# Kernel optimization log

Hardware: AMD Instinct MI355X
Metric: run time of the kernel (lower is better)

The kernel has to match this reference:

```python
import jax, jax.numpy as jnp
import numpy as np

B, T, N, D, H, C = 32, 64, 22, 512, 8, 128
DEPTH = D // H


def setup_inputs() -> dict:
    key = jax.random.key(0)
    ks = jax.random.split(key, 10)
    s = 0.02
    return {
        "x": jax.random.normal(ks[0], (B, T, N, D), jnp.float32),
        "context": jax.random.normal(ks[1], (B, C, D), jnp.float32),
        "Wq": jax.random.normal(ks[2], (N, D, D), jnp.float32) * s,  # per-joint Q proj
        "bq": jax.random.normal(ks[3], (N, D), jnp.float32) * s,
        "Wk": jax.random.normal(ks[4], (D, D), jnp.float32) * s,
        "bk": jax.random.normal(ks[5], (D,), jnp.float32) * s,
        "Wv": jax.random.normal(ks[6], (D, D), jnp.float32) * s,
        "bv": jax.random.normal(ks[7], (D,), jnp.float32) * s,
        "Wout": jax.random.normal(ks[8], (D, D), jnp.float32) * s,
        "bout": jax.random.normal(ks[9], (D,), jnp.float32) * s,
    }


def reference(x, context, Wq, bq, Wk, bk, Wv, bv, Wout, bout):
    b, t, n, d = x.shape
    c = context.shape[1]
    h, dh = H, DEPTH
    # Per-joint Q projection fused into one batched GEMM: [B,T,N,D] x [N,D,D] -> [B,T,N,D]
    q = jnp.einsum('btnd,ndf->btnf', x, Wq) + bq  # bq broadcasts over (B,T)
    # Shared K/V computed ONCE (original recomputes per joint; math identical)
    k = context @ Wk + bk  # [B,C,D]
    v = context @ Wv + bv  # [B,C,D]
    # Split heads
    qh = q.reshape(b, t, n, h, dh)
    kh = k.reshape(b, c, h, dh)
    vh = v.reshape(b, c, h, dh)
    scale = 1.0 / float(np.sqrt(dh))
    # Attention logits per joint: [B,N,H,T,C]
    logits = jnp.einsum('btnhd,bchd->bnhtc', qh, kh) * scale
    attn = jax.nn.softmax(logits, axis=-1)
    # Attend shared V, merge heads: [B,T,N,D]
    o = jnp.einsum('bnhtc,bchd->btnhd', attn, vh).reshape(b, t, n, d)
    # Shared output projection
    return o @ Wout + bout
```

## Files before the change

kernel.cpp:

```cpp
#include <hip/hip_runtime.h>
#include <hip/hip_bf16.h>

#define NB 32
#define NT 64
#define NJ 22
#define ND 512
#define NH 8
#define NC 128
#define NDH 64
#define NR 1408

typedef __attribute__((ext_vector_type(8))) short s16x8;
typedef __attribute__((ext_vector_type(4))) float fx4;

static __device__ __forceinline__ unsigned short f2bf(float f) {
    unsigned u = __builtin_bit_cast(unsigned, f);
    u += 0x7fffu + ((u >> 16) & 1u);
    return (unsigned short)(u >> 16);
}

static __device__ __forceinline__ fx4 mfma16(s16x8 a, s16x8 b, fx4 c) {
    return __builtin_amdgcn_mfma_f32_16x16x32_bf16(a, b, c, 0, 0, 0);
}

static __device__ __forceinline__ void gload16(const void* g, void* l) {
    __builtin_amdgcn_global_load_lds(
        (const __attribute__((address_space(1))) void*)g,
        (__attribute__((address_space(3))) void*)l,
        16, 0, 0);
}

template <int DIV>
__global__ __launch_bounds__(256) void convswz_k(const float* __restrict__ src,
                                                 unsigned short* __restrict__ dst)
{
    const long i = ((long)blockIdx.x * 256 + threadIdx.x) * 8;
    const unsigned row = (unsigned)(i >> 9);
    const int  key = (int)((row / (unsigned)DIV) & 7u);
    const int  c   = (int)((i >> 3) & 7);
    const int  cs  = c ^ key;
    const long j   = (i & ~63L) | ((long)cs << 3);
    const float4 a = *reinterpret_cast<const float4*>(src + i);
    const float4 b = *reinterpret_cast<const float4*>(src + i + 4);
    unsigned short t[8];
    t[0]=f2bf(a.x); t[1]=f2bf(a.y); t[2]=f2bf(a.z); t[3]=f2bf(a.w);
    t[4]=f2bf(b.x); t[5]=f2bf(b.y); t[6]=f2bf(b.z); t[7]=f2bf(b.w);
    *reinterpret_cast<s16x8*>(dst + j) = *reinterpret_cast<s16x8*>(t);
}

__global__ __launch_bounds__(256) void twconv_k(const float* __restrict__ W,
                                                unsigned short* __restrict__ Wt,
                                                long zsrc, long zdst)
{
    __shared__ float T[64][65];
    const int tid = threadIdx.x;
    W  += blockIdx.z * zsrc + (long)blockIdx.x * 64 * 512 + blockIdx.y * 64;
    Wt += blockIdx.z * zdst + (long)blockIdx.y * 64 * 512 + blockIdx.x * 64;
    const int r = tid >> 2, c0 = (tid & 3) * 16;
    #pragma unroll
    for (int i = 0; i < 4; ++i) {
        const float4 p = *reinterpret_cast<const float4*>(W + (long)r * 512 + c0 + i*4);
        T[r][c0 + i*4 + 0] = p.x; T[r][c0 + i*4 + 1] = p.y;
        T[r][c0 + i*4 + 2] = p.z; T[r][c0 + i*4 + 3] = p.w;
    }
    __syncthreads();
    unsigned short o[16];
    #pragma unroll
    for (int i = 0; i < 16; ++i) o[i] = f2bf(T[c0 + i][r]);
    const int ch0 = ((c0 >> 3) ^ (r & 7));
    *reinterpret_cast<s16x8*>(Wt + (long)r * 512 + ch0*8)       = *reinterpret_cast<s16x8*>(o);
    *reinterpret_cast<s16x8*>(Wt + (long)r * 512 + (ch0^1)*8)   = *reinterpret_cast<s16x8*>(o + 8);
}

template <typename TC, int MODE>
__global__ __launch_bounds__(256) void gemm128_k(
    const unsigned short* __restrict__ A, long lda,
    const unsigned short* __restrict__ Bt,
    const float* __restrict__ bias,
    TC* __restrict__ C, long ldc,
    long jsA, long jsW, long jsB, long jsC)
{
    __shared__ unsigned short As[2][128*64];
    __shared__ unsigned short Bs[2][128*64];

    const int tid = threadIdx.x;
    const int w = tid >> 6, lane = tid & 63;
    const long j = blockIdx.z;

    const int nx = gridDim.x;
    const int nwg = nx * gridDim.y;
    int lin = blockIdx.y * nx + blockIdx.x;
    lin = (lin & 7) * (nwg >> 3) + (lin >> 3);
    const int bx = lin % nx, by = lin / nx;

    A    += (long)bx * 128 * lda + j * jsA;
    Bt   += j * jsW + (long)by * 128 * 512;
    bias += j * jsB + by * 128;
    if constexpr (MODE == 0)
        C += (long)bx * 128 * ldc + j * jsC + by * 128;

    const int srow = lane >> 3;
    const int scol = (lane & 7) * 8;
    const unsigned short* Ag = A  + (long)(w*8 + srow) * lda + scol;
    const unsigned short* Bg = Bt + (long)(w*8 + srow) * 512 + scol;

    const int lr = lane & 15, lk = lane >> 4;
    const int wm = w >> 1, wn = w & 1;

    fx4 acc[4][4] = {};

    auto STAGE = [&](int buf, int kt) {
        char* Al = (char*)&As[buf][0] + w * 1024;
        char* Bl = (char*)&Bs[buf][0] + w * 1024;
        #pragma unroll
        for (int it = 0; it < 4; ++it)
            gload16(Ag + (long)it * 32 * lda + kt, Al + it * 4096);
        #pragma unroll
        for (int it = 0; it < 4; ++it)
            gload16(Bg + (long)it * 32 * 512 + kt, Bl + it * 4096);
    };

    auto COMPUTE = [&](int buf) {
        #pragma unroll
        for (int ks = 0; ks < 2; ++ks) {
            const int cha = (ks*4 + lk) ^ (lr & 7);
            s16x8 a[4], b[4];
            #pragma unroll
            for (int m = 0; m < 4; ++m)
                a[m] = *reinterpret_cast<const s16x8*>(&As[buf][(wm*64 + m*16 + lr)*64 + cha*8]);
            #pragma unroll
            for (int n = 0; n < 4; ++n)
                b[n] = *reinterpret_cast<const s16x8*>(&Bs[buf][(wn*64 + n*16 + lr)*64 + cha*8]);
            #pragma unroll
            for (int m = 0; m < 4; ++m)
                #pragma unroll
                for (int n = 0; n < 4; ++n)
                    acc[m][n] = mfma16(a[m], b[n], acc[m][n]);
        }
    };

    STAGE(0, 0);
    __syncthreads();
    #pragma unroll
    for (int t = 0; t < 7; ++t) {
        const int cur = t & 1;
        STAGE(cur ^ 1, (t + 1) * 64);
        COMPUTE(cur);
        __syncthreads();
    }
    COMPUTE(1);

    #pragma unroll
    for (int n = 0; n < 4; ++n) {
        const int col = wn*64 + n*16 + lr;
        const float bv = bias[col];
        #pragma unroll
        for (int m = 0; m < 4; ++m) {
            #pragma unroll
            for (int r = 0; r < 4; ++r) {
                const int row = wm*64 + m*16 + lk*4 + r;
                const float val = acc[m][n][r] + bv;
                if constexpr (MODE == 0) {
                    if constexpr (sizeof(TC) == 2)
                        reinterpret_cast<unsigned short*>(C)[(long)row*ldc + col] = f2bf(val);
                    else
                        reinterpret_cast<float*>(C)[(long)row*ldc + col] = val;
                } else {
                    const int grow = bx*128 + row;
                    const int gcol = by*128 + col;
                    const int b = grow >> 7, c = grow & 127;
                    const int hh = gcol >> 6, dh = gcol & 63;
                    unsigned short* Cp = reinterpret_cast<unsigned short*>(C);
                    if constexpr (MODE == 1) {
                        const int dhs = (dh & 7) | ((((dh >> 3) ^ (c & 7)) & 7) << 3);
                        Cp[(((long)b*8 + hh)*128 + c)*64 + dhs] = f2bf(val);
                    } else {
                        const int cs = (c & 7) | ((((c >> 3) ^ (dh & 7)) & 15) << 3);
                        Cp[(((long)b*8 + hh)*64 + dh)*128 + cs] = f2bf(val);
                    }
                }
            }
        }
    }
}

__global__ __launch_bounds__(256, 4) void attn3_k(
    const unsigned short* __restrict__ q,
    const unsigned short* __restrict__ kt,
    const unsigned short* __restrict__ vt,
    unsigned short* __restrict__ o)
{
    __shared__ __align__(16) unsigned short smem[20480];
    unsigned short* Qs = smem;
    unsigned short* Ks = smem + 4096;
    unsigned short* Vs = smem + 12288;

    const int tid = threadIdx.x;
    const int w = tid >> 6, lane = tid & 63;
    const int lr = lane & 15, lk = lane >> 4;
    const int r0 = blockIdx.x * 64;
    const int h = blockIdx.y;
    const int b = blockIdx.z;

    const unsigned short* qg = q + ((long)b*NR + r0 + w*16 + (lane>>3))*512
                                 + h*64 + (lane & 7)*8;
    const unsigned short* kg = kt + ((long)(b*8+h))*8192 + w*2048 + lane*8;
    const unsigned short* vg = vt + ((long)(b*8+h))*8192 + w*2048 + lane*8;

    gload16(qg,            (char*)Qs + w*2048);
    gload16(qg + 8*512,    (char*)Qs + w*2048 + 1024);
    #pragma unroll
    for (int it = 0; it < 4; ++it) {
        gload16(kg + it*512, (char*)Ks + w*4096 + it*1024);
        gload16(vg + it*512, (char*)Vs + w*4096 + it*1024);
    }
    __syncthreads();

    s16x8 aq[2];
    #pragma unroll
    for (int kk = 0; kk < 2; ++kk)
        aq[kk] = *reinterpret_cast<const s16x8*>(&Qs[(w*16 + lr)*64 + kk*32 + lk*8]);

    fx4 s[8] = {};
    #pragma unroll
    for (int kk = 0; kk < 2; ++kk) {
        #pragma unroll
        for (int f = 0; f < 8; ++f) {
            const int c = f*16 + lr;
            const int chunk = (kk*4 + lk) ^ (c & 7);
            s16x8 bk = *reinterpret_cast<const s16x8*>(&Ks[c*64 + chunk*8]);
            s[f] = mfma16(aq[kk], bk, s[f]);
        }
    }
    __syncthreads();

    unsigned short* P = Ks;

    const float SC = 0.125f * 1.44269504088896340736f;
    #pragma unroll
    for (int rr = 0; rr < 4; ++rr) {
        const int row = w*16 + lk*4 + rr;
        float mx = -3.0e38f;
        #pragma unroll
        for (int f = 0; f < 8; ++f) mx = fmaxf(mx, s[f][rr]);
        #pragma unroll
        for (int off = 1; off < 16; off <<= 1) mx = fmaxf(mx, __shfl_xor(mx, off));
        float p[8]; float sum = 0.f;
        #pragma unroll
        for (int f = 0; f < 8; ++f) {
            p[f] = exp2f((s[f][rr] - mx) * SC);
            sum += p[f];
        }
        #pragma unroll
        for (int off = 1; off < 16; off <<= 1) sum += __shfl_xor(sum, off);
        const float inv = 1.0f / sum;
        #pragma unroll
        for (int f = 0; f < 8; ++f) {
            const int cg = f*16 + lr;
            P[row*128 + (((cg >> 3) ^ (row & 7)) << 3) + (cg & 7)] = f2bf(p[f] * inv);
        }
    }

    fx4 oacc[4] = {};
    #pragma unroll
    for (int kt4 = 0; kt4 < 4; ++kt4) {
        const int prow = w*16 + lr;
        s16x8 ap = *reinterpret_cast<const s16x8*>(
            &P[prow*128 + (((kt4*4 + lk) ^ (prow & 7)) << 3)]);
        #pragma unroll
        for (int bn = 0; bn < 4; ++bn) {
            const int dh = bn*16 + lr;
            const int chunk = (kt4*4 + lk) ^ (dh & 7);
            s16x8 bv = *reinterpret_cast<const s16x8*>(&Vs[dh*128 + chunk*8]);
            oacc[bn] = mfma16(ap, bv, oacc[bn]);
        }
    }

    unsigned short* ob = o + ((long)b*NR + r0)*512 + h*64;
    #pragma unroll
    for (int bn = 0; bn < 4; ++bn)
        #pragma unroll
        for (int rr = 0; rr < 4; ++rr) {
            const int row = w*16 + lk*4 + rr;
            const int colg = bn*16 + lr;
            const int ch = ((colg >> 3) ^ (row & 7));
            ob[(long)row*512 + ch*8 + (lr & 7)] = f2bf(oacc[bn][rr]);
        }
}

extern "C" void kernel_launch(void* const* d_in, const int* in_sizes, int n_in,
                              void* d_out, int out_size, void* d_ws, size_t ws_size,
                              hipStream_t stream)
{
    const float* x    = (const float*)d_in[0];
    const float* ctx  = (const float*)d_in[1];
    const float* Wq   = (const float*)d_in[2];
    const float* bq   = (const float*)d_in[3];
    const float* Wk   = (const float*)d_in[4];
    const float* bk   = (const float*)d_in[5];
    const float* Wv   = (const float*)d_in[6];
    const float* bv   = (const float*)d_in[7];
    const float* Wout = (const float*)d_in[8];
    const float* bout = (const float*)d_in[9];
    float* out = (float*)d_out;

    const size_t NX  = (size_t)45056 * 512;
    const size_t NKV = (size_t)4096 * 512;
    const size_t NW  = (size_t)512 * 512;

    unsigned short* xbf   = (unsigned short*)d_ws;
    unsigned short* qbf   = xbf   + NX;
    unsigned short* cbf   = qbf   + NX;
    unsigned short* ktp   = cbf   + NKV;
    unsigned short* vtp   = ktp   + NKV;
    unsigned short* WqT   = vtp   + NKV;
    unsigned short* WkT   = WqT   + 22 * NW;
    unsigned short* WvT   = WkT   + NW;
    unsigned short* WoutT = WvT   + NW;
    unsigned short* obf   = xbf;

    convswz_k<NJ><<<dim3(NX / 2048), 256, 0, stream>>>(x, xbf);
    convswz_k<1><<<dim3(NKV / 2048), 256, 0, stream>>>(ctx, cbf);
    twconv_k<<<dim3(8, 8, 22), 256, 0, stream>>>(Wq,   WqT,   (long)NW, (long)NW);
    twconv_k<<<dim3(8, 8, 1),  256, 0, stream>>>(Wk,   WkT,   0, 0);
    twconv_k<<<dim3(8, 8, 1),  256, 0, stream>>>(Wv,   WvT,   0, 0);
    twconv_k<<<dim3(8, 8, 1),  256, 0, stream>>>(Wout, WoutT, 0, 0);

    gemm128_k<unsigned short, 0><<<dim3(16, 4, NJ), 256, 0, stream>>>(
        xbf, (long)NJ*ND, WqT, bq, qbf, (long)NJ*ND,
        (long)ND, (long)NW, (long)ND, (long)ND);

    gemm128_k<unsigned short, 1><<<dim3(32, 4, 1), 256, 0, stream>>>(
        cbf, ND, WkT, bk, ktp, ND, 0, 0, 0, 0);
    gemm128_k<unsigned short, 2><<<dim3(32, 4, 1), 256, 0, stream>>>(
        cbf, ND, WvT, bv, vtp, ND, 0, 0, 0, 0);

    attn3_k<<<dim3(NR/64, NH, NB), 256, 0, stream>>>(qbf, ktp, vtp, obf);

    gemm128_k<float, 0><<<dim3(45056/128, 4, 1), 256, 0, stream>>>(
        obf, ND, WoutT, bout, out, ND, 0, 0, 0, 0);
}
```

Before: 200.6 us.

## Fuse fp32-to-bf16 conversion of x and context into GEMM A-tile loads

Drops the standalone conversion kernels for x and context. The Q, K and V GEMMs now read the fp32 activations directly into registers, convert them to bf16 and write them into swizzled LDS, with the global loads issued before the MFMA compute to overlap latency. This removes one full write and re-read of the bf16 copy of x (about 92 MB fp32 read plus 46 MB bf16 traffic). The trade-off is that each A element is read as fp32 by the four N-blocks that share it, which doubles A bytes per block. The GEMM also takes on register-staged loads and extra VALU conversion work.

```diff
diff --git a/kernel.cpp b/kernel.cpp
--- a/kernel.cpp
+++ b/kernel.cpp
@@ -28,24 +28,6 @@
         (const __attribute__((address_space(1))) void*)g,
         (__attribute__((address_space(3))) void*)l,
         16, 0, 0);
-}
-
-template <int DIV>
-__global__ __launch_bounds__(256) void convswz_k(const float* __restrict__ src,
-                                                 unsigned short* __restrict__ dst)
-{
-    const long i = ((long)blockIdx.x * 256 + threadIdx.x) * 8;
-    const unsigned row = (unsigned)(i >> 9);
-    const int  key = (int)((row / (unsigned)DIV) & 7u);
-    const int  c   = (int)((i >> 3) & 7);
-    const int  cs  = c ^ key;
-    const long j   = (i & ~63L) | ((long)cs << 3);
-    const float4 a = *reinterpret_cast<const float4*>(src + i);
-    const float4 b = *reinterpret_cast<const float4*>(src + i + 4);
-    unsigned short t[8];
-    t[0]=f2bf(a.x); t[1]=f2bf(a.y); t[2]=f2bf(a.z); t[3]=f2bf(a.w);
-    t[4]=f2bf(b.x); t[5]=f2bf(b.y); t[6]=f2bf(b.z); t[7]=f2bf(b.w);
-    *reinterpret_cast<s16x8*>(dst + j) = *reinterpret_cast<s16x8*>(t);
 }
 
 __global__ __launch_bounds__(256) void twconv_k(const float* __restrict__ W,
@@ -72,9 +54,9 @@
     *reinterpret_cast<s16x8*>(Wt + (long)r * 512 + (ch0^1)*8)   = *reinterpret_cast<s16x8*>(o + 8);
 }
 
-template <typename TC, int MODE>
+template <typename TC, int MODE, bool AF32>
 __global__ __launch_bounds__(256) void gemm128_k(
-    const unsigned short* __restrict__ A, long lda,
+    const void* __restrict__ Av, long lda,
     const unsigned short* __restrict__ Bt,
     const float* __restrict__ bias,
     TC* __restrict__ C, long ldc,
@@ -93,7 +75,6 @@
     lin = (lin & 7) * (nwg >> 3) + (lin >> 3);
     const int bx = lin % nx, by = lin / nx;
 
-    A    += (long)bx * 128 * lda + j * jsA;
     Bt   += j * jsW + (long)by * 128 * 512;
     bias += j * jsB + by * 128;
     if constexpr (MODE == 0)
@@ -101,23 +82,50 @@
 
     const int srow = lane >> 3;
     const int scol = (lane & 7) * 8;
-    const unsigned short* Ag = A  + (long)(w*8 + srow) * lda + scol;
+    const long aoff = (long)bx * 128 * lda + j * jsA + (long)(w*8 + srow) * lda + scol;
+    const float*          Ag32 = (const float*)Av + aoff;
+    const unsigned short* Ag16 = (const unsigned short*)Av + aoff;
     const unsigned short* Bg = Bt + (long)(w*8 + srow) * 512 + scol;
 
     const int lr = lane & 15, lk = lane >> 4;
     const int wm = w >> 1, wn = w & 1;
+    const int achunk = (lane & 7) ^ srow;
 
     fx4 acc[4][4] = {};
-
-    auto STAGE = [&](int buf, int kt) {
-        char* Al = (char*)&As[buf][0] + w * 1024;
+    float4 ra[4][2];
+
+    auto STAGE_B = [&](int buf, int kt) {
         char* Bl = (char*)&Bs[buf][0] + w * 1024;
-        #pragma unroll
-        for (int it = 0; it < 4; ++it)
-            gload16(Ag + (long)it * 32 * lda + kt, Al + it * 4096);
         #pragma unroll
         for (int it = 0; it < 4; ++it)
             gload16(Bg + (long)it * 32 * 512 + kt, Bl + it * 4096);
+    };
+    auto STAGE_A_LDS = [&](int buf, int kt) {
+        char* Al = (char*)&As[buf][0] + w * 1024;
+        #pragma unroll
+        for (int it = 0; it < 4; ++it)
+            gload16(Ag16 + (long)it * 32 * lda + kt, Al + it * 4096);
+    };
+    auto A_LOAD = [&](int kt) {
+        #pragma unroll
+        for (int it = 0; it < 4; ++it) {
+            const float* p = Ag32 + (long)it * 32 * lda + kt;
+            ra[it][0] = *reinterpret_cast<const float4*>(p);
+            ra[it][1] = *reinterpret_cast<const float4*>(p + 4);
+        }
+    };
+    auto A_WRITE = [&](int buf) {
+        #pragma unroll
+        for (int it = 0; it < 4; ++it) {
+            unsigned short t[8];
+            t[0]=f2bf(ra[it][0].x); t[1]=f2bf(ra[it][0].y);
+            t[2]=f2bf(ra[it][0].z); t[3]=f2bf(ra[it][0].w);
+            t[4]=f2bf(ra[it][1].x); t[5]=f2bf(ra[it][1].y);
+            t[6]=f2bf(ra[it][1].z); t[7]=f2bf(ra[it][1].w);
+            *reinterpret_cast<s16x8*>(
+                &As[buf][(it*32 + w*8 + srow)*64 + achunk*8]) =
+                *reinterpret_cast<s16x8*>(t);
+        }
     };
 
     auto COMPUTE = [&](int buf) {
@@ -139,13 +147,30 @@
         }
     };
 
-    STAGE(0, 0);
+    if constexpr (AF32) {
+        A_LOAD(0);
+        STAGE_B(0, 0);
+        A_WRITE(0);
+    } else {
+        STAGE_A_LDS(0, 0);
+        STAGE_B(0, 0);
+    }
     __syncthreads();
+
     #pragma unroll
     for (int t = 0; t < 7; ++t) {
         const int cur = t & 1;
-        STAGE(cur ^ 1, (t + 1) * 64);
-        COMPUTE(cur);
+        const int kt_next = (t + 1) * 64;
+        if constexpr (AF32) {
+            A_LOAD(kt_next);
+            STAGE_B(cur ^ 1, kt_next);
+            COMPUTE(cur);
+            A_WRITE(cur ^ 1);
+        } else {
+            STAGE_A_LDS(cur ^ 1, kt_next);
+            STAGE_B(cur ^ 1, kt_next);
+            COMPUTE(cur);
+        }
         __syncthreads();
     }
     COMPUTE(1);
@@ -308,35 +333,31 @@
     const size_t NKV = (size_t)4096 * 512;
     const size_t NW  = (size_t)512 * 512;
 
-    unsigned short* xbf   = (unsigned short*)d_ws;
-    unsigned short* qbf   = xbf   + NX;
-    unsigned short* cbf   = qbf   + NX;
-    unsigned short* ktp   = cbf   + NKV;
+    unsigned short* qbf   = (unsigned short*)d_ws;
+    unsigned short* obf   = qbf   + NX;
+    unsigned short* ktp   = obf   + NX;
     unsigned short* vtp   = ktp   + NKV;
     unsigned short* WqT   = vtp   + NKV;
     unsigned short* WkT   = WqT   + 22 * NW;
     unsigned short* WvT   = WkT   + NW;
     unsigned short* WoutT = WvT   + NW;
-    unsigned short* obf   = xbf;
-
-    convswz_k<NJ><<<dim3(NX / 2048), 256, 0, stream>>>(x, xbf);
-    convswz_k<1><<<dim3(NKV / 2048), 256, 0, stream>>>(ctx, cbf);
+
     twconv_k<<<dim3(8, 8, 22), 256, 0, stream>>>(Wq,   WqT,   (long)NW, (long)NW);
     twconv_k<<<dim3(8, 8, 1),  256, 0, stream>>>(Wk,   WkT,   0, 0);
     twconv_k<<<dim3(8, 8, 1),  256, 0, stream>>>(Wv,   WvT,   0, 0);
     twconv_k<<<dim3(8, 8, 1),  256, 0, stream>>>(Wout, WoutT, 0, 0);
 
-    gemm128_k<unsigned short, 0><<<dim3(16, 4, NJ), 256, 0, stream>>>(
-        xbf, (long)NJ*ND, WqT, bq, qbf, (long)NJ*ND,
+    gemm128_k<unsigned short, 0, true><<<dim3(16, 4, NJ), 256, 0, stream>>>(
+        x, (long)NJ*ND, WqT, bq, qbf, (long)NJ*ND,
         (long)ND, (long)NW, (long)ND, (long)ND);
 
-    gemm128_k<unsigned short, 1><<<dim3(32, 4, 1), 256, 0, stream>>>(
-        cbf, ND, WkT, bk, ktp, ND, 0, 0, 0, 0);
-    gemm128_k<unsigned short, 2><<<dim3(32, 4, 1), 256, 0, stream>>>(
-        cbf, ND, WvT, bv, vtp, ND, 0, 0, 0, 0);
+    gemm128_k<unsigned short, 1, true><<<dim3(32, 4, 1), 256, 0, stream>>>(
+        ctx, ND, WkT, bk, ktp, ND, 0, 0, 0, 0);
+    gemm128_k<unsigned short, 2, true><<<dim3(32, 4, 1), 256, 0, stream>>>(
+        ctx, ND, WvT, bv, vtp, ND, 0, 0, 0, 0);
 
     attn3_k<<<dim3(NR/64, NH, NB), 256, 0, stream>>>(qbf, ktp, vtp, obf);
 
-    gemm128_k<float, 0><<<dim3(45056/128, 4, 1), 256, 0, stream>>>(
+    gemm128_k<float, 0, false><<<dim3(45056/128, 4, 1), 256, 0, stream>>>(
         obf, ND, WoutT, bout, out, ND, 0, 0, 0, 0);
 }
```

After: 210.1 us. 4.7% more time.
